# Performance work log

Measured on AMD Instinct MI355X. Metric: run time of the kernel, lower is better.

Reference implementation:

```python
import jax, jax.numpy as jnp
import numpy as np

B, C, T, H, W = 8, 512, 8, 32, 32
CI = C // 2  # inter_channels
EPS = 1e-5


def _conv1x1(x, w, b):
    # x: (b, c, t, h, w); w: (o, c); b: (o,)
    return jnp.einsum('bcthw,oc->bothw', x, w) + b[None, :, None, None, None]


def _maxpool2(v):
    # MaxPool3d(kernel=2, stride=2) on (t, h, w)
    b, c, t, h, w = v.shape
    return v.reshape(b, c, t // 2, 2, h // 2, 2, w // 2, 2).max(axis=(3, 5, 7))


def setup_inputs() -> dict:
    key = jax.random.key(0)
    ks = jax.random.split(key, 12)
    s = 0.02
    return {
        'x': jax.random.normal(ks[0], (B, C, T, H, W), dtype=jnp.float32),
        'theta_w': jax.random.normal(ks[1], (CI, C), dtype=jnp.float32) * s,
        'theta_b': jnp.zeros((CI,), dtype=jnp.float32),
        'phi_w': jax.random.normal(ks[2], (CI, C), dtype=jnp.float32) * s,
        'phi_b': jnp.zeros((CI,), dtype=jnp.float32),
        'g_w': jax.random.normal(ks[3], (CI, C), dtype=jnp.float32) * s,
        'g_b': jnp.zeros((CI,), dtype=jnp.float32),
        'wz_w': jax.random.normal(ks[4], (C, CI), dtype=jnp.float32) * s,
        'wz_b': jnp.zeros((C,), dtype=jnp.float32),
        'bn_gamma': jax.random.uniform(ks[5], (C,), dtype=jnp.float32, minval=0.5, maxval=1.5),
        'bn_beta': jax.random.normal(ks[6], (C,), dtype=jnp.float32) * 0.1,
    }


def reference(x, theta_w, theta_b, phi_w, phi_b, g_w, g_b, wz_w, wz_b, bn_gamma, bn_beta):
    b = x.shape[0]
    # projections (1x1x1 convs == channel matmuls)
    theta_x = _conv1x1(x, theta_w, theta_b)            # (b, ci, t, h, w)
    phi_x = _maxpool2(_conv1x1(x, phi_w, phi_b))       # (b, ci, t/2, h/2, w/2)
    g_x = _maxpool2(_conv1x1(x, g_w, g_b))             # (b, ci, t/2, h/2, w/2)

    ci = theta_x.shape[1]
    q = theta_x.reshape(b, ci, -1).transpose(0, 2, 1)  # (b, N, ci)
    k = phi_x.reshape(b, ci, -1)                       # (b, ci, M)
    v = g_x.reshape(b, ci, -1).transpose(0, 2, 1)      # (b, M, ci)

    f = jnp.einsum('bnc,bcm->bnm', q, k)               # (b, N, M)
    attn = jax.nn.softmax(f, axis=-1)                  # embedded_gaussian
    y = jnp.einsum('bnm,bmc->bnc', attn, v)            # (b, N, ci)
    y = y.transpose(0, 2, 1).reshape(b, ci, *x.shape[2:])

    # Wz: 1x1x1 conv + BatchNorm3d (training-mode batch stats, eps=1e-5)
    z = _conv1x1(y, wz_w, wz_b)                        # (b, C, t, h, w)
    mean = z.mean(axis=(0, 2, 3, 4), keepdims=True)
    var = z.var(axis=(0, 2, 3, 4), keepdims=True)
    z = (z - mean) * jax.lax.rsqrt(var + EPS)
    z = z * bn_gamma[None, :, None, None, None] + bn_beta[None, :, None, None, None]
    return z + x
```

## Files before the change

### kernel.cpp

```cpp
#include <hip/hip_runtime.h>
#include <math.h>

typedef unsigned short u16;
typedef __attribute__((ext_vector_type(8))) _Float16 half8;
typedef __attribute__((ext_vector_type(4))) float f32x4;

#define NS 8192
#define MS 1024
#define CCH 512
#define CI 256
#define O3 768

__device__ __forceinline__ float h2f(u16 u) {
    _Float16 h; *(u16*)&h = u; return (float)h;
}
__device__ __forceinline__ u16 f2h(float f) {
    _Float16 h = (_Float16)f; return *(u16*)&h;
}

__device__ __forceinline__ void gld16(u16* lds, const u16* g) {
    __builtin_amdgcn_global_load_lds((const __attribute__((address_space(1))) void*)g,
                                     (__attribute__((address_space(3))) void*)lds,
                                     16, 0, 0);
}

__global__ void prep_w(const float* __restrict__ tw, const float* __restrict__ tb,
                       const float* __restrict__ pw, const float* __restrict__ pb,
                       const float* __restrict__ gw, const float* __restrict__ gb,
                       const float* __restrict__ wzw,
                       u16* __restrict__ W3b, float* __restrict__ b3, u16* __restrict__ wzb) {
    int i = blockIdx.x * 256 + threadIdx.x;
    if (i < O3 * CCH) {
        int o = i >> 9, c = i & 511;
        float v = (o < 256) ? tw[o * 512 + c] : (o < 512) ? pw[(o - 256) * 512 + c]
                                              : gw[(o - 512) * 512 + c];
        W3b[i] = f2h(v);
    } else {
        int j = i - O3 * CCH;
        if (j < CCH * CI) wzb[j] = f2h(wzw[j]);
    }
    if (i < O3) b3[i] = (i < 256) ? tb[i] : (i < 512) ? pb[i - 256] : gb[i - 512];
}

__global__ __launch_bounds__(256) void transpose_x(const float* __restrict__ x,
                                                   u16* __restrict__ xt) {
    __shared__ float tile[64][129];
    int b = blockIdx.z;
    int n0 = blockIdx.x * 128, c0 = blockIdx.y * 64;
    const float* xb = x + ((size_t)b * CCH + c0) * NS + n0;
    int t = threadIdx.x;
    #pragma unroll
    for (int i = 0; i < 32; ++i) {
        int idx = t + i * 256;
        int c = idx >> 7, n = idx & 127;
        tile[c][n] = xb[(size_t)c * NS + n];
    }
    __syncthreads();
    u16* xo = xt + ((size_t)b * NS + n0) * CCH + c0;
    #pragma unroll
    for (int i = 0; i < 16; ++i) {
        int idx = t + i * 256;
        int cp = idx & 31, n = idx >> 5;
        unsigned lo = f2h(tile[2 * cp][n]);
        unsigned hi = f2h(tile[2 * cp + 1][n]);
        *(unsigned*)(xo + (size_t)n * CCH + 2 * cp) = lo | (hi << 16);
    }
}

template<int BIAS_MODE>
__global__ __launch_bounds__(256) void gemm_nt_f16(
        const u16* __restrict__ A, const u16* __restrict__ Bm,
        u16* __restrict__ C, const float* __restrict__ bias,
        int lda, int ldb, int ldc, int Ksize,
        size_t strideA, size_t strideB, size_t strideC) {
    __shared__ u16 As[2][128 * 64];
    __shared__ u16 Bs[2][128 * 64];
    const int t = threadIdx.x;
    const int l = t & 63, w = t >> 6;
    const int wr = w >> 1, wc = w & 1;
    const int fr = l & 15, fq = l >> 4;

    const int nx = gridDim.x, ny = gridDim.y;
    int bid = blockIdx.x + nx * (blockIdx.y + ny * blockIdx.z);
    int cpx = (nx * ny * (int)gridDim.z) >> 3;
    int Wd = (bid & 7) * cpx + (bid >> 3);
    int bx = Wd % nx, rem = Wd / nx;
    int by = rem % ny, bz = rem / ny;

    const u16* gA = A + (size_t)bz * strideA + (size_t)(by * 128) * lda;
    const u16* gB = Bm + (size_t)bz * strideB + (size_t)(bx * 128) * ldb;

    f32x4 acc[4][4];
    #pragma unroll
    for (int m = 0; m < 4; ++m)
        #pragma unroll
        for (int n = 0; n < 4; ++n) acc[m][n] = (f32x4)0.f;

    #define STAGE_AB(buf, k0)                                                 \
        {                                                                     \
            _Pragma("unroll")                                                 \
            for (int i = 0; i < 4; ++i) {                                     \
                int cd = t + i * 256;                                         \
                int row = cd >> 3;                                            \
                int k8 = ((cd & 7) ^ (row & 7)) * 8;                          \
                int lbase = (cd & ~63) * 8;                                   \
                gld16(&As[buf][lbase], gA + (size_t)row * lda + (k0) + k8);   \
                gld16(&Bs[buf][lbase], gB + (size_t)row * ldb + (k0) + k8);   \
            }                                                                 \
        }

    const int nk = Ksize >> 6;
    STAGE_AB(0, 0);
    STAGE_AB(1, 64);

    for (int mt = 0; mt < nk; ++mt) {
        const int cur = mt & 1;
        if (mt == nk - 1) asm volatile("s_waitcnt vmcnt(0)" ::: "memory");
        else              asm volatile("s_waitcnt vmcnt(8)" ::: "memory");
        __builtin_amdgcn_sched_barrier(0);
        __builtin_amdgcn_s_barrier();

        half8 fa[4][2], fb[4][2];
        #pragma unroll
        for (int m = 0; m < 4; ++m)
            #pragma unroll
            for (int kk = 0; kk < 2; ++kk) {
                int ra = wr * 64 + m * 16 + fr;
                int rb = wc * 64 + m * 16 + fr;
                fa[m][kk] = *(const half8*)&As[cur][ra * 64 + ((((kk << 2) | fq)) ^ (ra & 7)) * 8];
                fb[m][kk] = *(const half8*)&Bs[cur][rb * 64 + ((((kk << 2) | fq)) ^ (rb & 7)) * 8];
            }
        __builtin_amdgcn_s_setprio(1);
        #pragma unroll
        for (int kk = 0; kk < 2; ++kk)
            #pragma unroll
            for (int m = 0; m < 4; ++m)
                #pragma unroll
                for (int n = 0; n < 4; ++n)
                    acc[m][n] = __builtin_amdgcn_mfma_f32_16x16x32_f16(
                        fa[m][kk], fb[n][kk], acc[m][n], 0, 0, 0);
        __builtin_amdgcn_s_setprio(0);

        __builtin_amdgcn_s_barrier();
        if (mt + 2 < nk) STAGE_AB(cur, (mt + 2) * 64);
    }
    #undef STAGE_AB

    u16* gC = C + (size_t)bz * strideC;
    const int crow0 = by * 128 + wr * 64;
    const int ccol0 = bx * 128 + wc * 64;
    #pragma unroll
    for (int m = 0; m < 4; ++m) {
        #pragma unroll
        for (int n = 0; n < 4; ++n) {
            int col = ccol0 + n * 16 + fr;
            float cb = (BIAS_MODE == 2) ? bias[col] : 0.f;
            #pragma unroll
            for (int j = 0; j < 4; ++j) {
                int row = crow0 + m * 16 + fq * 4 + j;
                float v = acc[m][n][j] + cb;
                if (BIAS_MODE == 1) v += bias[row];
                gC[(size_t)row * ldc + col] = f2h(v);
            }
        }
    }
}

__global__ __launch_bounds__(256) void pool_kernel(const u16* __restrict__ proj,
                                                   u16* __restrict__ kb, u16* __restrict__ vg) {
    int tid = blockIdx.x * 256 + threadIdx.x;
    int b = tid >> 18;
    int m = (tid >> 8) & 1023;
    int ci = tid & 255;
    int tp = m >> 8, hp = (m >> 4) & 15, wp = m & 15;
    const u16* pb = proj + (size_t)b * NS * O3;
    float mk = -1e30f, mv = -1e30f;
    #pragma unroll
    for (int d = 0; d < 8; ++d) {
        int dt = d >> 2, dh = (d >> 1) & 1, dw = d & 1;
        int n = (2 * tp + dt) * 1024 + (2 * hp + dh) * 32 + (2 * wp + dw);
        const u16* r = pb + (size_t)n * O3;
        mk = fmaxf(mk, h2f(r[256 + ci]));
        mv = fmaxf(mv, h2f(r[512 + ci]));
    }
    kb[((size_t)b * MS + m) * CI + ci] = f2h(mk);
    vg[((size_t)b * CI + ci) * MS + m] = f2h(mv);
}

__global__ __launch_bounds__(512, 2) void attn_fused(
        const u16* __restrict__ proj, const u16* __restrict__ kb,
        const u16* __restrict__ vg, u16* __restrict__ y) {
    __shared__ u16 Ks[2][64 * 256];
    __shared__ u16 Vs[2][256 * 64];
    __shared__ u16 Ps[8][16][40];

    int bid0 = blockIdx.x + 64 * blockIdx.y;
    int W = (bid0 & 7) * 64 + (bid0 >> 3);
    const int b = W >> 6;
    const int n0 = (W & 63) * 128;

    const int t = threadIdx.x;
    const int l = t & 63, w = t >> 6;
    const int fr = l & 15, fq = l >> 4;

    const u16* projb = proj + (size_t)b * NS * O3;
    const u16* kbb = kb + (size_t)b * MS * CI;
    const u16* vgb = vg + (size_t)b * CI * MS;

    half8 qf[8];
    {
        const u16* qrow = projb + (size_t)(n0 + w * 16 + fr) * O3 + fq * 8;
        #pragma unroll
        for (int kk = 0; kk < 8; ++kk)
            qf[kk] = *(const half8*)(qrow + kk * 32);
    }

    f32x4 accO[16];
    #pragma unroll
    for (int nf = 0; nf < 16; ++nf) accO[nf] = (f32x4)0.f;
    float m_run[4], l_run[4];
    #pragma unroll
    for (int j = 0; j < 4; ++j) { m_run[j] = -1e30f; l_run[j] = 0.f; }

    #define STAGE_KV(buf, m0)                                                     \
        {                                                                         \
            _Pragma("unroll")                                                     \
            for (int i = 0; i < 4; ++i) {                                         \
                int c = t + i * 512;                                              \
                int lb = (c & ~63) << 3;                                          \
                int krow = c >> 5, kk8 = c & 31;                                  \
                gld16(&Ks[buf][lb],                                               \
                      kbb + (size_t)((m0) + krow) * CI + ((kk8 ^ (krow & 7)) << 3)); \
                int vrow = c >> 3, vk8 = c & 7;                                   \
                gld16(&Vs[buf][lb],                                               \
                      vgb + (size_t)vrow * MS + (m0) + ((vk8 ^ (vrow & 7)) << 3)); \
            }                                                                     \
        }

    STAGE_KV(0, 0);
    STAGE_KV(1, 64);

    for (int mt = 0; mt < 16; ++mt) {
        const int cur = mt & 1;
        if (mt == 15) asm volatile("s_waitcnt vmcnt(0)" ::: "memory");
        else          asm volatile("s_waitcnt vmcnt(8)" ::: "memory");
        __builtin_amdgcn_sched_barrier(0);
        __builtin_amdgcn_s_barrier();

        f32x4 accS[4];
        #pragma unroll
        for (int nf = 0; nf < 4; ++nf) accS[nf] = (f32x4)0.f;
        __builtin_amdgcn_s_setprio(1);
        #pragma unroll
        for (int kk = 0; kk < 8; ++kk) {
            half8 fb[4];
            #pragma unroll
            for (int nf = 0; nf < 4; ++nf) {
                int row = nf * 16 + fr;
                fb[nf] = *(const half8*)&Ks[cur][row * 256 + (((kk << 2) | fq) ^ (row & 7)) * 8];
            }
            #pragma unroll
            for (int nf = 0; nf < 4; ++nf)
                accS[nf] = __builtin_amdgcn_mfma_f32_16x16x32_f16(
                    qf[kk], fb[nf], accS[nf], 0, 0, 0);
        }
        __builtin_amdgcn_s_setprio(0);

        float pm[4];
        #pragma unroll
        for (int j = 0; j < 4; ++j)
            pm[j] = fmaxf(fmaxf(accS[0][j], accS[1][j]),
                          fmaxf(accS[2][j], accS[3][j]));
        #pragma unroll
        for (int off = 1; off < 16; off <<= 1)
            #pragma unroll
            for (int j = 0; j < 4; ++j)
                pm[j] = fmaxf(pm[j], __shfl_xor(pm[j], off));

        int chg = 0;
        #pragma unroll
        for (int j = 0; j < 4; ++j) chg |= (pm[j] > m_run[j]);
        if (__any(chg)) {
            #pragma unroll
            for (int j = 0; j < 4; ++j) {
                float mn = fmaxf(m_run[j], pm[j]);
                float a = __expf(m_run[j] - mn);
                m_run[j] = mn;
                l_run[j] *= a;
                #pragma unroll
                for (int nf = 0; nf < 16; ++nf) accO[nf][j] *= a;
            }
        }

        #pragma unroll
        for (int kkm = 0; kkm < 2; ++kkm) {
            #pragma unroll
            for (int j = 0; j < 4; ++j) {
                float ps = 0.f;
                #pragma unroll
                for (int nfh = 0; nfh < 2; ++nfh) {
                    float p = __expf(accS[kkm * 2 + nfh][j] - m_run[j]);
                    ps += p;
                    Ps[w][fq * 4 + j][nfh * 16 + fr] = f2h(p);
                }
                #pragma unroll
                for (int off = 1; off < 16; off <<= 1) ps += __shfl_xor(ps, off);
                l_run[j] += ps;
            }
            half8 fa = *(const half8*)&Ps[w][fr][fq * 8];
            __builtin_amdgcn_s_setprio(1);
            #pragma unroll
            for (int nf = 0; nf < 16; ++nf) {
                int row = nf * 16 + fr;
                half8 fbv = *(const half8*)&Vs[cur][row * 64 + (((kkm << 2) | fq) ^ (row & 7)) * 8];
                accO[nf] = __builtin_amdgcn_mfma_f32_16x16x32_f16(
                    fa, fbv, accO[nf], 0, 0, 0);
            }
            __builtin_amdgcn_s_setprio(0);
        }

        __builtin_amdgcn_s_barrier();
        if (mt < 14) STAGE_KV(cur, (mt + 2) * 64);
    }

    u16* yb = y + ((size_t)b * NS + n0 + w * 16) * CI;
    #pragma unroll
    for (int j = 0; j < 4; ++j) {
        float inv = 1.f / l_run[j];
        int row = fq * 4 + j;
        #pragma unroll
        for (int nf = 0; nf < 16; ++nf)
            yb[(size_t)row * CI + nf * 16 + fr] = f2h(accO[nf][j] * inv);
    }
    #undef STAGE_KV
}

__global__ __launch_bounds__(256) void bn_stats(const u16* __restrict__ z,
                                                float* __restrict__ stats) {
    int c = blockIdx.x, t = threadIdx.x;
    float s = 0.f, q = 0.f;
    for (int b = 0; b < 8; ++b) {
        const u16* p = z + ((size_t)b * CCH + c) * NS;
        #pragma unroll
        for (int i = 0; i < 4; ++i) {
            uint4 v = *(const uint4*)(p + (t + i * 256) * 8);
            const u16* u = (const u16*)&v;
            #pragma unroll
            for (int j = 0; j < 8; ++j) { float f = h2f(u[j]); s += f; q += f * f; }
        }
    }
    #pragma unroll
    for (int off = 32; off; off >>= 1) { s += __shfl_xor(s, off); q += __shfl_xor(q, off); }
    __shared__ float rs[4], rq[4];
    int w = t >> 6;
    if ((t & 63) == 0) { rs[w] = s; rq[w] = q; }
    __syncthreads();
    if (t == 0) {
        float S2 = rs[0] + rs[1] + rs[2] + rs[3];
        float Q = rq[0] + rq[1] + rq[2] + rq[3];
        const float inv = 1.f / 65536.f;
        float mean = S2 * inv;
        float var = Q * inv - mean * mean;
        stats[c] = mean;
        stats[CCH + c] = rsqrtf(var + 1e-5f);
    }
}

__global__ __launch_bounds__(256) void bn_final(const u16* __restrict__ z,
                                                const float* __restrict__ x,
                                                const float* __restrict__ stats,
                                                const float* __restrict__ gamma,
                                                const float* __restrict__ beta,
                                                float* __restrict__ out) {
    size_t i = ((size_t)blockIdx.x * 256 + threadIdx.x) * 8;
    int c = (int)((i >> 13) & 511);
    float g = gamma[c] * stats[CCH + c];
    float sh = beta[c] - stats[c] * g;
    uint4 zv = *(const uint4*)(z + i);
    const u16* u = (const u16*)&zv;
    float4 x0 = *(const float4*)(x + i);
    float4 x1 = *(const float4*)(x + i + 4);
    float4 o0, o1;
    o0.x = h2f(u[0]) * g + sh + x0.x;
    o0.y = h2f(u[1]) * g + sh + x0.y;
    o0.z = h2f(u[2]) * g + sh + x0.z;
    o0.w = h2f(u[3]) * g + sh + x0.w;
    o1.x = h2f(u[4]) * g + sh + x1.x;
    o1.y = h2f(u[5]) * g + sh + x1.y;
    o1.z = h2f(u[6]) * g + sh + x1.z;
    o1.w = h2f(u[7]) * g + sh + x1.w;
    *(float4*)(out + i) = o0;
    *(float4*)(out + i + 4) = o1;
}

extern "C" void kernel_launch(void* const* d_in, const int* in_sizes, int n_in,
                              void* d_out, int out_size, void* d_ws, size_t ws_size,
                              hipStream_t stream) {
    const float* x       = (const float*)d_in[0];
    const float* theta_w = (const float*)d_in[1];
    const float* theta_b = (const float*)d_in[2];
    const float* phi_w   = (const float*)d_in[3];
    const float* phi_b   = (const float*)d_in[4];
    const float* g_w     = (const float*)d_in[5];
    const float* g_b     = (const float*)d_in[6];
    const float* wz_w    = (const float*)d_in[7];
    const float* wz_b    = (const float*)d_in[8];
    const float* gamma   = (const float*)d_in[9];
    const float* beta    = (const float*)d_in[10];

    char* base = (char*)d_ws;
    u16*   W3b  = (u16*)base;
    float* b3   = (float*)(base + 786432);
    u16*   wzb  = (u16*)(base + 789504);
    float* stats= (float*)(base + 1051648);
    u16* xt   = (u16*)(base + 1056768);
    u16* kb   = xt;
    u16* vg   = xt + (size_t)8 * MS * CI;
    u16* z    = xt;
    u16* proj = (u16*)(base + 1056768 + 67108864);
    u16* y    = (u16*)(base + 1056768 + 67108864 + 100663296);

    prep_w<<<2048, 256, 0, stream>>>(theta_w, theta_b, phi_w, phi_b, g_w, g_b,
                                     wz_w, W3b, b3, wzb);
    transpose_x<<<dim3(64, 8, 8), 256, 0, stream>>>(x, xt);

    gemm_nt_f16<2><<<dim3(6, 64, 8), 256, 0, stream>>>(
        xt, W3b, proj, b3, CCH, CCH, O3, CCH,
        (size_t)NS * CCH, 0, (size_t)NS * O3);

    pool_kernel<<<8192, 256, 0, stream>>>(proj, kb, vg);

    attn_fused<<<dim3(64, 8), 512, 0, stream>>>(proj, kb, vg, y);

    gemm_nt_f16<1><<<dim3(64, 4, 8), 256, 0, stream>>>(
        wzb, y, z, wz_b, CI, CI, NS, CI,
        0, (size_t)NS * CI, (size_t)CCH * NS);

    bn_stats<<<CCH, 256, 0, stream>>>(z, stats);

    bn_final<<<16384, 256, 0, stream>>>(z, x, stats, gamma, beta, (float*)d_out);
}
```

Measured before the change: 383.2 us.

## Fuse spatial maxpool into projection GEMM epilogue and offload softmax row ops

The projection GEMM now writes theta to a compact buffer and applies the 2x2 spatial max-pool to phi/g directly in registers, storing a quarter-size intermediate. A lighter pool2 kernel then does only the temporal pairwise max. This avoids writing and re-reading the full phi/g projection. In attention, the cross-lane row max uses DPP instead of shuffles, and the softmax row sum is computed with an MFMA against a ones vector rather than shuffle reductions. The row sum now accumulates from fp16-rounded probabilities, and the workspace layout is larger.

```diff
diff --git a/kernel.cpp b/kernel.cpp
--- a/kernel.cpp
+++ b/kernel.cpp
@@ -22,6 +22,21 @@
     __builtin_amdgcn_global_load_lds((const __attribute__((address_space(1))) void*)g,
                                      (__attribute__((address_space(3))) void*)lds,
                                      16, 0, 0);
+}
+
+template<int CTRL>
+__device__ __forceinline__ float dppmax(float x) {
+    union { float f; int i; } a, b;
+    a.f = x;
+    b.i = __builtin_amdgcn_update_dpp(a.i, a.i, CTRL, 0xF, 0xF, false);
+    return fmaxf(a.f, b.f);
+}
+__device__ __forceinline__ float rowmax16(float x) {
+    x = dppmax<0xB1>(x);
+    x = dppmax<0x4E>(x);
+    x = dppmax<0x141>(x);
+    x = dppmax<0x140>(x);
+    return x;
 }
 
 __global__ void prep_w(const float* __restrict__ tw, const float* __restrict__ tb,
@@ -67,6 +82,138 @@
     }
 }
 
+__global__ __launch_bounds__(256) void proj_gemm(
+        const u16* __restrict__ A, const u16* __restrict__ Bm,
+        const float* __restrict__ bias,
+        u16* __restrict__ projq, u16* __restrict__ P1) {
+    __shared__ u16 As[2][128 * 64];
+    __shared__ u16 Bs[2][128 * 64];
+    const int t = threadIdx.x;
+    const int l = t & 63, w = t >> 6;
+    const int wr = w >> 1, wc = w & 1;
+    const int fr = l & 15, fq = l >> 4;
+
+    const int nx = gridDim.x, ny = gridDim.y;
+    int bid = blockIdx.x + nx * (blockIdx.y + ny * blockIdx.z);
+    int cpx = (nx * ny * (int)gridDim.z) >> 3;
+    int Wd = (bid & 7) * cpx + (bid >> 3);
+    int bx = Wd % nx, rem = Wd / nx;
+    int by = rem % ny, bz = rem / ny;
+
+    const u16* gA = A + (size_t)bz * NS * CCH + (size_t)(by * 128) * CCH;
+    const u16* gB = Bm + (size_t)(bx * 128) * CCH;
+
+    f32x4 acc[4][4];
+    #pragma unroll
+    for (int m = 0; m < 4; ++m)
+        #pragma unroll
+        for (int n = 0; n < 4; ++n) acc[m][n] = (f32x4)0.f;
+
+    #define STAGE_AB(buf, k0)                                                 \
+        {                                                                     \
+            _Pragma("unroll")                                                 \
+            for (int i = 0; i < 4; ++i) {                                     \
+                int cd = t + i * 256;                                         \
+                int row = cd >> 3;                                            \
+                int k8 = ((cd & 7) ^ (row & 7)) * 8;                          \
+                int lbase = (cd & ~63) * 8;                                   \
+                gld16(&As[buf][lbase], gA + (size_t)row * CCH + (k0) + k8);   \
+                gld16(&Bs[buf][lbase], gB + (size_t)row * CCH + (k0) + k8);   \
+            }                                                                 \
+        }
+
+    const int nk = CCH >> 6;
+    STAGE_AB(0, 0);
+    STAGE_AB(1, 64);
+
+    for (int mt = 0; mt < nk; ++mt) {
+        const int cur = mt & 1;
+        if (mt == nk - 1) asm volatile("s_waitcnt vmcnt(0)" ::: "memory");
+        else              asm volatile("s_waitcnt vmcnt(8)" ::: "memory");
+        __builtin_amdgcn_sched_barrier(0);
+        __builtin_amdgcn_s_barrier();
+
+        half8 fa[4][2], fb[4][2];
+        #pragma unroll
+        for (int m = 0; m < 4; ++m)
+            #pragma unroll
+            for (int kk = 0; kk < 2; ++kk) {
+                int ra = wr * 64 + m * 16 + fr;
+                int rb = wc * 64 + m * 16 + fr;
+                fa[m][kk] = *(const half8*)&As[cur][ra * 64 + ((((kk << 2) | fq)) ^ (ra & 7)) * 8];
+                fb[m][kk] = *(const half8*)&Bs[cur][rb * 64 + ((((kk << 2) | fq)) ^ (rb & 7)) * 8];
+            }
+        __builtin_amdgcn_s_setprio(1);
+        #pragma unroll
+        for (int kk = 0; kk < 2; ++kk)
+            #pragma unroll
+            for (int m = 0; m < 4; ++m)
+                #pragma unroll
+                for (int n = 0; n < 4; ++n)
+                    acc[m][n] = __builtin_amdgcn_mfma_f32_16x16x32_f16(
+                        fa[m][kk], fb[n][kk], acc[m][n], 0, 0, 0);
+        __builtin_amdgcn_s_setprio(0);
+
+        __builtin_amdgcn_s_barrier();
+        if (mt + 2 < nk) STAGE_AB(cur, (mt + 2) * 64);
+    }
+    #undef STAGE_AB
+
+    const int ccol0 = bx * 128 + wc * 64;
+    if (ccol0 < 256) {
+        u16* gC = projq + (size_t)bz * NS * 256;
+        const int crow0 = by * 128 + wr * 64;
+        #pragma unroll
+        for (int m = 0; m < 4; ++m)
+            #pragma unroll
+            for (int n = 0; n < 4; ++n) {
+                int col = ccol0 + n * 16 + fr;
+                float cb = bias[col];
+                #pragma unroll
+                for (int j = 0; j < 4; ++j) {
+                    int row = crow0 + m * 16 + fq * 4 + j;
+                    gC[(size_t)row * 256 + col] = f2h(acc[m][n][j] + cb);
+                }
+            }
+    } else {
+        int tt = by >> 3;
+        int h2 = ((by & 7) << 1) + wr;
+        u16* gP = P1 + ((size_t)bz * 2048 + tt * 256 + h2 * 16) * 512;
+        #pragma unroll
+        for (int mh = 0; mh < 2; ++mh)
+            #pragma unroll
+            for (int n = 0; n < 4; ++n) {
+                int col = ccol0 + n * 16 + fr;
+                float cb = bias[col];
+                int c1 = col - 256;
+                #pragma unroll
+                for (int jj = 0; jj < 2; ++jj) {
+                    float mx = fmaxf(
+                        fmaxf(acc[mh][n][2 * jj], acc[mh][n][2 * jj + 1]),
+                        fmaxf(acc[mh + 2][n][2 * jj], acc[mh + 2][n][2 * jj + 1]));
+                    int w2 = mh * 8 + fq * 2 + jj;
+                    gP[(size_t)w2 * 512 + c1] = f2h(mx + cb);
+                }
+            }
+    }
+}
+
+__global__ __launch_bounds__(256) void pool2_kernel(const u16* __restrict__ P1,
+                                                    u16* __restrict__ kb,
+                                                    u16* __restrict__ vg) {
+    int tid = blockIdx.x * 256 + threadIdx.x;
+    int b = tid >> 18;
+    int m = (tid >> 8) & 1023;
+    int ci = tid & 255;
+    int tp = m >> 8, hw = m & 255;
+    const u16* p0 = P1 + ((size_t)b * 2048 + (2 * tp) * 256 + hw) * 512;
+    const u16* p1 = p0 + 256 * 512;
+    float k = fmaxf(h2f(p0[ci]), h2f(p1[ci]));
+    float v = fmaxf(h2f(p0[256 + ci]), h2f(p1[256 + ci]));
+    kb[((size_t)b * MS + m) * CI + ci] = f2h(k);
+    vg[((size_t)b * CI + ci) * MS + m] = f2h(v);
+}
+
 template<int BIAS_MODE>
 __global__ __launch_bounds__(256) void gemm_nt_f16(
         const u16* __restrict__ A, const u16* __restrict__ Bm,
@@ -166,29 +313,8 @@
     }
 }
 
-__global__ __launch_bounds__(256) void pool_kernel(const u16* __restrict__ proj,
-                                                   u16* __restrict__ kb, u16* __restrict__ vg) {
-    int tid = blockIdx.x * 256 + threadIdx.x;
-    int b = tid >> 18;
-    int m = (tid >> 8) & 1023;
-    int ci = tid & 255;
-    int tp = m >> 8, hp = (m >> 4) & 15, wp = m & 15;
-    const u16* pb = proj + (size_t)b * NS * O3;
-    float mk = -1e30f, mv = -1e30f;
-    #pragma unroll
-    for (int d = 0; d < 8; ++d) {
-        int dt = d >> 2, dh = (d >> 1) & 1, dw = d & 1;
-        int n = (2 * tp + dt) * 1024 + (2 * hp + dh) * 32 + (2 * wp + dw);
-        const u16* r = pb + (size_t)n * O3;
-        mk = fmaxf(mk, h2f(r[256 + ci]));
-        mv = fmaxf(mv, h2f(r[512 + ci]));
-    }
-    kb[((size_t)b * MS + m) * CI + ci] = f2h(mk);
-    vg[((size_t)b * CI + ci) * MS + m] = f2h(mv);
-}
-
 __global__ __launch_bounds__(512, 2) void attn_fused(
-        const u16* __restrict__ proj, const u16* __restrict__ kb,
+        const u16* __restrict__ projq, const u16* __restrict__ kb,
         const u16* __restrict__ vg, u16* __restrict__ y) {
     __shared__ u16 Ks[2][64 * 256];
     __shared__ u16 Vs[2][256 * 64];
@@ -203,24 +329,29 @@
     const int l = t & 63, w = t >> 6;
     const int fr = l & 15, fq = l >> 4;
 
-    const u16* projb = proj + (size_t)b * NS * O3;
+    const u16* projb = projq + (size_t)b * NS * 256;
     const u16* kbb = kb + (size_t)b * MS * CI;
     const u16* vgb = vg + (size_t)b * CI * MS;
 
     half8 qf[8];
     {
-        const u16* qrow = projb + (size_t)(n0 + w * 16 + fr) * O3 + fq * 8;
+        const u16* qrow = projb + (size_t)(n0 + w * 16 + fr) * 256 + fq * 8;
         #pragma unroll
         for (int kk = 0; kk < 8; ++kk)
             qf[kk] = *(const half8*)(qrow + kk * 32);
     }
 
+    half8 ones;
+    #pragma unroll
+    for (int i = 0; i < 8; ++i) ones[i] = (_Float16)1.f;
+
     f32x4 accO[16];
     #pragma unroll
     for (int nf = 0; nf < 16; ++nf) accO[nf] = (f32x4)0.f;
-    float m_run[4], l_run[4];
-    #pragma unroll
-    for (int j = 0; j < 4; ++j) { m_run[j] = -1e30f; l_run[j] = 0.f; }
+    f32x4 accL = (f32x4)0.f;
+    float m_run[4];
+    #pragma unroll
+    for (int j = 0; j < 4; ++j) m_run[j] = -1e30f;
 
     #define STAGE_KV(buf, m0)                                                     \
         {                                                                         \
@@ -269,13 +400,8 @@
         float pm[4];
         #pragma unroll
         for (int j = 0; j < 4; ++j)
-            pm[j] = fmaxf(fmaxf(accS[0][j], accS[1][j]),
-                          fmaxf(accS[2][j], accS[3][j]));
-        #pragma unroll
-        for (int off = 1; off < 16; off <<= 1)
-            #pragma unroll
-            for (int j = 0; j < 4; ++j)
-                pm[j] = fmaxf(pm[j], __shfl_xor(pm[j], off));
+            pm[j] = rowmax16(fmaxf(fmaxf(accS[0][j], accS[1][j]),
+                                   fmaxf(accS[2][j], accS[3][j])));
 
         int chg = 0;
         #pragma unroll
@@ -286,7 +412,7 @@
                 float mn = fmaxf(m_run[j], pm[j]);
                 float a = __expf(m_run[j] - mn);
                 m_run[j] = mn;
-                l_run[j] *= a;
+                accL[j] *= a;
                 #pragma unroll
                 for (int nf = 0; nf < 16; ++nf) accO[nf][j] *= a;
             }
@@ -295,19 +421,14 @@
         #pragma unroll
         for (int kkm = 0; kkm < 2; ++kkm) {
             #pragma unroll
-            for (int j = 0; j < 4; ++j) {
-                float ps = 0.f;
+            for (int j = 0; j < 4; ++j)
                 #pragma unroll
                 for (int nfh = 0; nfh < 2; ++nfh) {
                     float p = __expf(accS[kkm * 2 + nfh][j] - m_run[j]);
-                    ps += p;
                     Ps[w][fq * 4 + j][nfh * 16 + fr] = f2h(p);
                 }
-                #pragma unroll
-                for (int off = 1; off < 16; off <<= 1) ps += __shfl_xor(ps, off);
-                l_run[j] += ps;
-            }
             half8 fa = *(const half8*)&Ps[w][fr][fq * 8];
+            accL = __builtin_amdgcn_mfma_f32_16x16x32_f16(fa, ones, accL, 0, 0, 0);
             __builtin_amdgcn_s_setprio(1);
             #pragma unroll
             for (int nf = 0; nf < 16; ++nf) {
@@ -326,7 +447,7 @@
     u16* yb = y + ((size_t)b * NS + n0 + w * 16) * CI;
     #pragma unroll
     for (int j = 0; j < 4; ++j) {
-        float inv = 1.f / l_run[j];
+        float inv = 1.f / accL[j];
         int row = fq * 4 + j;
         #pragma unroll
         for (int nf = 0; nf < 16; ++nf)
@@ -409,28 +530,27 @@
     const float* beta    = (const float*)d_in[10];
 
     char* base = (char*)d_ws;
-    u16*   W3b  = (u16*)base;
-    float* b3   = (float*)(base + 786432);
-    u16*   wzb  = (u16*)(base + 789504);
-    float* stats= (float*)(base + 1051648);
-    u16* xt   = (u16*)(base + 1056768);
-    u16* kb   = xt;
-    u16* vg   = xt + (size_t)8 * MS * CI;
-    u16* z    = xt;
-    u16* proj = (u16*)(base + 1056768 + 67108864);
-    u16* y    = (u16*)(base + 1056768 + 67108864 + 100663296);
+    u16*   W3b   = (u16*)base;
+    float* b3    = (float*)(base + 786432);
+    u16*   wzb   = (u16*)(base + 789504);
+    float* stats = (float*)(base + 1051648);
+    u16*   projq = (u16*)(base + 1056768);
+    u16*   P1    = (u16*)(base + 1056768 + 33554432);
+    u16*   kb    = (u16*)(base + 1056768 + 50331648);
+    u16*   vg    = (u16*)(base + 1056768 + 54525952);
+    u16*   xt    = (u16*)(base + 1056768 + 58720256);
+    u16*   y     = (u16*)(base + 1056768 + 125829120);
+    u16*   z     = (u16*)(base + 1056768 + 159383552);
 
     prep_w<<<2048, 256, 0, stream>>>(theta_w, theta_b, phi_w, phi_b, g_w, g_b,
                                      wz_w, W3b, b3, wzb);
     transpose_x<<<dim3(64, 8, 8), 256, 0, stream>>>(x, xt);
 
-    gemm_nt_f16<2><<<dim3(6, 64, 8), 256, 0, stream>>>(
-        xt, W3b, proj, b3, CCH, CCH, O3, CCH,
-        (size_t)NS * CCH, 0, (size_t)NS * O3);
-
-    pool_kernel<<<8192, 256, 0, stream>>>(proj, kb, vg);
-
-    attn_fused<<<dim3(64, 8), 512, 0, stream>>>(proj, kb, vg, y);
+    proj_gemm<<<dim3(6, 64, 8), 256, 0, stream>>>(xt, W3b, b3, projq, P1);
+
+    pool2_kernel<<<8192, 256, 0, stream>>>(P1, kb, vg);
+
+    attn_fused<<<dim3(64, 8), 512, 0, stream>>>(projq, kb, vg, y);
 
     gemm_nt_f16<1><<<dim3(64, 4, 8), 256, 0, stream>>>(
         wzb, y, z, wz_b, CI, CI, NS, CI,
```

Result: faster. 346.2 us (-9.6%).
